# Optimization experiments

Hardware: AMD Instinct MI355X
Metric: run time of the kernel (lower is better)

The kernel has to match this reference:

```python
import jax, jax.numpy as jnp
import numpy as np
from jax import lax

B, T, E, H, V, D_ACT, OUT = 128, 512, 12, 512, 16, 10, 64


def setup_inputs() -> dict:
    key = jax.random.key(0)
    ks = jax.random.split(key, 9)
    ts = jax.random.uniform(ks[0], (B, T, 2), dtype=jnp.float32)
    idx = jax.random.randint(ks[1], (B, T), 0, V).astype(jnp.float32)
    x = jnp.concatenate([ts, idx[..., None]], axis=-1)  # [B,T,3], col2 = activity ids
    emb = jax.random.normal(ks[2], (V, D_ACT), jnp.float32) * 0.1
    emb = emb.at[0].set(0.0)  # padding_idx=0
    W_fwd = jax.random.normal(ks[3], (E, 3 * H), jnp.float32) / np.sqrt(E).astype(np.float32)
    b_fwd = jnp.zeros((3 * H,), jnp.float32)
    W_bwd = jax.random.normal(ks[4], (E, 3 * H), jnp.float32) / np.sqrt(E).astype(np.float32)
    b_bwd = jnp.zeros((3 * H,), jnp.float32)
    weight_Mu = jax.random.normal(ks[5], (2 * H, 1), jnp.float32) * 0.1
    W_out = jax.random.normal(ks[6], (OUT, 2 * H), jnp.float32) * 0.01  # torch Linear layout [out,in]
    b_out = jnp.zeros((OUT,), jnp.float32)
    return {"x": x, "emb": emb, "W_fwd": W_fwd, "b_fwd": b_fwd,
            "W_bwd": W_bwd, "b_bwd": b_bwd, "weight_Mu": weight_Mu,
            "W_out": W_out, "b_out": b_out}


def _fo_pool(z, f):
    # h_t = f_t * h_{t-1} + (1 - f_t) * z_t, scanned over time (axis 0)
    def step(c, zf):
        z_t, f_t = zf
        c = f_t * c + (1.0 - f_t) * z_t
        return c, c
    c0 = jnp.zeros_like(z[0])
    _, cs = lax.scan(step, c0, (z, f))
    return cs  # [T,B,H]


def _qrnn_dir(inp, W, b):
    # inp: [T,B,E] -> gates [T,B,3H]
    Y = inp @ W + b
    Z, F_, O = jnp.split(Y, 3, axis=-1)
    Z = jnp.tanh(Z)
    F_ = jax.nn.sigmoid(F_)
    O = jax.nn.sigmoid(O)
    C = _fo_pool(Z, F_)
    return O * C  # [T,B,H]


def reference(x, emb, W_fwd, b_fwd, W_bwd, b_bwd, weight_Mu, W_out, b_out):
    ts = x[:, :, :2]                                   # [B,T,2] time features
    act = emb[x[:, :, 2].astype(jnp.int32)]            # [B,T,10]
    enc = jnp.concatenate([ts, act], axis=-1)          # [B,T,E]
    inp = jnp.transpose(enc, (1, 0, 2))                # [T,B,E]
    h_f = _qrnn_dir(inp, W_fwd, b_fwd)                 # [T,B,H]
    h_b = _qrnn_dir(inp[::-1], W_bwd, b_bwd)[::-1]     # reverse-direction QRNN
    out = jnp.concatenate([h_f, h_b], axis=-1)         # [T,B,2H]
    out = jax.nn.relu(jnp.transpose(out, (1, 0, 2)))   # [B,T,2H]
    attn = jax.nn.softmax(out @ weight_Mu, axis=1)     # [B,T,1], softmax over time
    context = jnp.einsum('btd,bt->bd', out, attn[..., 0])  # [B,2H]
    context = jax.nn.relu(context)
    return context @ W_out.T + b_out                   # [B,OUT]
```

## Files before the change

kernel.cpp:

```cpp
#include <hip/hip_runtime.h>
#include <hip/hip_bf16.h>

#define B_   128
#define T_   512
#define H_   512
#define V_   16
#define OUT_ 64
#define DH_  1024


#define TAB_BYTES (V_*H_*16)
#define TSA_BYTES (T_*8)
#define VPK_BYTES (T_)
#define SCAN_LDS  (TAB_BYTES + TSA_BYTES + VPK_BYTES)

#define LOG2E 1.4426950408889634f

__device__ __forceinline__ float bf2f_lo(unsigned int u) {
    union { unsigned int i; float f; } x; x.i = u << 16; return x.f;
}
__device__ __forceinline__ float bf2f_hi(unsigned int u) {
    union { unsigned int i; float f; } x; x.i = u & 0xffff0000u; return x.f;
}

__global__ __launch_bounds__(512) void qrnn_scan8(
    const float* __restrict__ x,
    const float* __restrict__ emb,
    const float* __restrict__ Wf, const float* __restrict__ bf_,
    const float* __restrict__ Wb, const float* __restrict__ bb_,
    __hip_bfloat16* __restrict__ hbuf)
{
    const int b = blockIdx.x, dir = blockIdx.y, h = threadIdx.x;
    const float* __restrict__ W    = dir ? Wb  : Wf;
    const float* __restrict__ bias = dir ? bb_ : bf_;

    extern __shared__ char smem[];
    float4*        tab = (float4*)smem;
    float2*        tsA = (float2*)(smem + TAB_BYTES);
    unsigned char* vpk = (unsigned char*)(smem + TAB_BYTES + TSA_BYTES);

    {
        const int t = h;
        const float* xp = x + ((size_t)b*T_ + t)*3;
        tsA[t] = make_float2(xp[0], xp[1]);
        vpk[t] = (unsigned char)(int)xp[2];
    }

    float w0[3], w1[3], wt[10][3];
#pragma unroll
    for (int g = 0; g < 3; ++g) {
        w0[g] = W[g*H_ + h];
        w1[g] = W[1536 + g*H_ + h];
#pragma unroll
        for (int e = 0; e < 10; ++e)
            wt[e][g] = W[(2+e)*1536 + g*H_ + h];
    }
    const float bz = bias[h], bfv = bias[H_+h], bov = bias[2*H_+h];

    const float FZ = -2.8853900817779268f;
    const float FF = -1.4426950408889634f;

#pragma unroll
    for (int v = 0; v < V_; ++v) {
        float a0 = bz, a1 = bfv, a2 = bov;
#pragma unroll
        for (int e = 0; e < 10; ++e) {
            const float ev = emb[v*10 + e];
            a0 = fmaf(ev, wt[e][0], a0);
            a1 = fmaf(ev, wt[e][1], a1);
            a2 = fmaf(ev, wt[e][2], a2);
        }
        tab[v*H_ + h] = make_float4(FZ*a0, FF*a1, FF*a2, 0.f);
    }
    const float w0z = FZ*w0[0], w0f = FF*w0[1], w0o = FF*w0[2];
    const float w1z = FZ*w1[0], w1f = FF*w1[1], w1o = FF*w1[2];
    __syncthreads();

    const float4* tsA4 = (const float4*)tsA;
    const uint2*  vp2  = (const uint2*)vpk;

    float c = 0.f;
    __hip_bfloat16* hb = hbuf + (size_t)b*DH_ + dir*H_ + h;

#define SS(i, A0, A1, G) { \
    const float zp = fmaf(A0, w0z, fmaf(A1, w1z, (G).x)); \
    const float fp = fmaf(A0, w0f, fmaf(A1, w1f, (G).y)); \
    const float op = fmaf(A0, w0o, fmaf(A1, w1o, (G).z)); \
    const float Az = 1.f + __builtin_amdgcn_exp2f(zp); \
    const float Bf = 1.f + __builtin_amdgcn_exp2f(fp); \
    const float Co = 1.f + __builtin_amdgcn_exp2f(op); \
    const float AB = Az*Bf, BC = Bf*Co, AC = Az*Co; \
    const float r  = __builtin_amdgcn_rcpf(AB*Co); \
    const float f  = AC*r; \
    const float og = AB*r; \
    const float z  = (2.f - Az)*(BC*r); \
    c = fmaf(f, c - z, z); \
    const float hv = fmaxf(og * c, 0.f); \
    hb[(size_t)(t0 + (i))*(B_*DH_)] = __float2bfloat16(hv); \
}

#pragma unroll 2
    for (int gi = 0; gi < T_/8; ++gi) {
        const int gg = dir ? (T_/8 - 1 - gi) : gi;
        const int t0 = gg*8;
        const uint2  vp  = vp2[gg];
        const float4 tsa = tsA4[gg*4 + 0];
        const float4 tsb = tsA4[gg*4 + 1];
        const float4 tsc = tsA4[gg*4 + 2];
        const float4 tsd = tsA4[gg*4 + 3];
        const int v0 =  vp.x        & 255, v1 = (vp.x >> 8) & 255;
        const int v2 = (vp.x >> 16) & 255, v3 =  vp.x >> 24;
        const int v4 =  vp.y        & 255, v5 = (vp.y >> 8) & 255;
        const int v6 = (vp.y >> 16) & 255, v7 =  vp.y >> 24;
        const float4 g0 = tab[v0*H_ + h];
        const float4 g1 = tab[v1*H_ + h];
        const float4 g2 = tab[v2*H_ + h];
        const float4 g3 = tab[v3*H_ + h];
        const float4 g4 = tab[v4*H_ + h];
        const float4 g5 = tab[v5*H_ + h];
        const float4 g6 = tab[v6*H_ + h];
        const float4 g7 = tab[v7*H_ + h];
        if (dir == 0) {
            SS(0, tsa.x, tsa.y, g0) SS(1, tsa.z, tsa.w, g1)
            SS(2, tsb.x, tsb.y, g2) SS(3, tsb.z, tsb.w, g3)
            SS(4, tsc.x, tsc.y, g4) SS(5, tsc.z, tsc.w, g5)
            SS(6, tsd.x, tsd.y, g6) SS(7, tsd.z, tsd.w, g7)
        } else {
            SS(7, tsd.z, tsd.w, g7) SS(6, tsd.x, tsd.y, g6)
            SS(5, tsc.z, tsc.w, g5) SS(4, tsc.x, tsc.y, g4)
            SS(3, tsb.z, tsb.w, g3) SS(2, tsb.x, tsb.y, g2)
            SS(1, tsa.z, tsa.w, g1) SS(0, tsa.x, tsa.y, g0)
        }
    }
#undef SS
}

__global__ __launch_bounds__(1024) void postfuse(
    const __hip_bfloat16* __restrict__ hbuf,
    const float* __restrict__ Mu,
    const float* __restrict__ Wout,
    const float* __restrict__ bout,
    float* __restrict__ out)
{
    const int b    = blockIdx.x;
    const int w    = threadIdx.x >> 6;
    const int lane = threadIdx.x & 63;

    __shared__ float pw[16][DH_];
    __shared__ float psum[16];

    float mu[16];
    const float4* mp = (const float4*)Mu;
#pragma unroll
    for (int k = 0; k < 2; ++k) {
        const float4 m0 = mp[(k*64 + lane)*2];
        const float4 m1 = mp[(k*64 + lane)*2 + 1];
        mu[k*8+0]=m0.x; mu[k*8+1]=m0.y; mu[k*8+2]=m0.z; mu[k*8+3]=m0.w;
        mu[k*8+4]=m1.x; mu[k*8+5]=m1.y; mu[k*8+6]=m1.z; mu[k*8+7]=m1.w;
    }

    float acc[16];
#pragma unroll
    for (int i = 0; i < 16; ++i) acc[i] = 0.f;
    float esum = 0.f;

    for (int j = 0; j < T_/16; ++j) {
        const int t = j*16 + w;
        const uint4* hp = (const uint4*)(hbuf + ((size_t)t*B_ + b)*DH_);
        const uint4 u0 = hp[lane];
        const uint4 u1 = hp[64 + lane];
        float hv[16];
        hv[0]  = bf2f_lo(u0.x); hv[1]  = bf2f_hi(u0.x);
        hv[2]  = bf2f_lo(u0.y); hv[3]  = bf2f_hi(u0.y);
        hv[4]  = bf2f_lo(u0.z); hv[5]  = bf2f_hi(u0.z);
        hv[6]  = bf2f_lo(u0.w); hv[7]  = bf2f_hi(u0.w);
        hv[8]  = bf2f_lo(u1.x); hv[9]  = bf2f_hi(u1.x);
        hv[10] = bf2f_lo(u1.y); hv[11] = bf2f_hi(u1.y);
        hv[12] = bf2f_lo(u1.z); hv[13] = bf2f_hi(u1.z);
        hv[14] = bf2f_lo(u1.w); hv[15] = bf2f_hi(u1.w);

        float s = 0.f;
#pragma unroll
        for (int i = 0; i < 16; ++i) s = fmaf(hv[i], mu[i], s);
#pragma unroll
        for (int off = 1; off <= 32; off <<= 1) s += __shfl_xor(s, off);

        const float e = __builtin_amdgcn_exp2f(s * LOG2E);
        esum += e;
#pragma unroll
        for (int i = 0; i < 16; ++i) acc[i] = fmaf(hv[i], e, acc[i]);
    }

#pragma unroll
    for (int k = 0; k < 2; ++k) {
        *(float4*)&pw[w][k*512 + lane*8]     = make_float4(acc[k*8+0], acc[k*8+1], acc[k*8+2], acc[k*8+3]);
        *(float4*)&pw[w][k*512 + lane*8 + 4] = make_float4(acc[k*8+4], acc[k*8+5], acc[k*8+6], acc[k*8+7]);
    }
    if (lane == 0) psum[w] = esum;
    __syncthreads();

    {
        const int d = threadIdx.x;
        float cs = 0.f;
#pragma unroll
        for (int i = 0; i < 16; ++i) cs += pw[i][d];
        pw[0][d] = fmaxf(cs, 0.f);
    }
    float rsum = 0.f;
#pragma unroll
    for (int i = 0; i < 16; ++i) rsum += psum[i];
    const float rinv = __builtin_amdgcn_rcpf(rsum);
    __syncthreads();

#pragma unroll
    for (int oo = 0; oo < 4; ++oo) {
        const int o = w*4 + oo;
        const float* wp = Wout + o*DH_;
        float a = 0.f;
#pragma unroll
        for (int k = 0; k < 16; ++k) {
            const int d = k*64 + lane;
            a = fmaf(pw[0][d], wp[d], a);
        }
#pragma unroll
        for (int off = 1; off <= 32; off <<= 1) a += __shfl_xor(a, off);
        if (lane == 0) out[b*OUT_ + o] = a*rinv + bout[o];
    }
}

extern "C" void kernel_launch(void* const* d_in, const int* in_sizes, int n_in,
                              void* d_out, int out_size, void* d_ws, size_t ws_size,
                              hipStream_t stream)
{
    const float* x    = (const float*)d_in[0];
    const float* emb  = (const float*)d_in[1];
    const float* Wf   = (const float*)d_in[2];
    const float* bf_  = (const float*)d_in[3];
    const float* Wb   = (const float*)d_in[4];
    const float* bb_  = (const float*)d_in[5];
    const float* Mu   = (const float*)d_in[6];
    const float* Wout = (const float*)d_in[7];
    const float* bout = (const float*)d_in[8];
    float* out = (float*)d_out;

    __hip_bfloat16* hbuf = (__hip_bfloat16*)d_ws;

    (void)hipFuncSetAttribute((const void*)qrnn_scan8,
                              hipFuncAttributeMaxDynamicSharedMemorySize,
                              SCAN_LDS);

    qrnn_scan8<<<dim3(B_, 2), 512, SCAN_LDS, stream>>>(x, emb, Wf, bf_, Wb, bb_, hbuf);
    postfuse<<<B_, 1024, 0, stream>>>(hbuf, Mu, Wout, bout, out);
}
```

Before: 172.0 us.

## Split attention pooling over time chunks and simplify gate activations with rcp

The attention/context pooling kernel now runs on a (batch, 8 time-chunk) grid of 512-thread blocks instead of one 1024-thread block per batch. Each block writes partial context sums and exp sums to workspace, and a new combine kernel reduces them and applies the output projection. This targets the poor occupancy of the old 128-block pooling launch, at the cost of an extra kernel launch and a partial-sum round trip through global memory. The scan kernel also replaces the shared-reciprocal sigmoid/tanh formulation with three separate rcp calls, trading extra transcendental ops for fewer multiplies.

```diff
diff --git a/kernel.cpp b/kernel.cpp
--- a/kernel.cpp
+++ b/kernel.cpp
@@ -7,6 +7,7 @@
 #define V_   16
 #define OUT_ 64
 #define DH_  1024
+#define NCH  8
 
 
 #define TAB_BYTES (V_*H_*16)
@@ -23,7 +24,7 @@
     union { unsigned int i; float f; } x; x.i = u & 0xffff0000u; return x.f;
 }
 
-__global__ __launch_bounds__(512) void qrnn_scan8(
+__global__ __launch_bounds__(512) void qrnn_scan9(
     const float* __restrict__ x,
     const float* __restrict__ emb,
     const float* __restrict__ Wf, const float* __restrict__ bf_,
@@ -86,16 +87,12 @@
     const float zp = fmaf(A0, w0z, fmaf(A1, w1z, (G).x)); \
     const float fp = fmaf(A0, w0f, fmaf(A1, w1f, (G).y)); \
     const float op = fmaf(A0, w0o, fmaf(A1, w1o, (G).z)); \
-    const float Az = 1.f + __builtin_amdgcn_exp2f(zp); \
-    const float Bf = 1.f + __builtin_amdgcn_exp2f(fp); \
-    const float Co = 1.f + __builtin_amdgcn_exp2f(op); \
-    const float AB = Az*Bf, BC = Bf*Co, AC = Az*Co; \
-    const float r  = __builtin_amdgcn_rcpf(AB*Co); \
-    const float f  = AC*r; \
-    const float og = AB*r; \
-    const float z  = (2.f - Az)*(BC*r); \
+    const float rz = __builtin_amdgcn_rcpf(1.f + __builtin_amdgcn_exp2f(zp)); \
+    const float f  = __builtin_amdgcn_rcpf(1.f + __builtin_amdgcn_exp2f(fp)); \
+    const float o  = __builtin_amdgcn_rcpf(1.f + __builtin_amdgcn_exp2f(op)); \
+    const float z  = fmaf(2.f, rz, -1.f); \
     c = fmaf(f, c - z, z); \
-    const float hv = fmaxf(og * c, 0.f); \
+    const float hv = fmaxf(o * c, 0.f); \
     hb[(size_t)(t0 + (i))*(B_*DH_)] = __float2bfloat16(hv); \
 }
 
@@ -135,19 +132,19 @@
 #undef SS
 }
 
-__global__ __launch_bounds__(1024) void postfuse(
+__global__ __launch_bounds__(512) void postfuse2(
     const __hip_bfloat16* __restrict__ hbuf,
     const float* __restrict__ Mu,
-    const float* __restrict__ Wout,
-    const float* __restrict__ bout,
-    float* __restrict__ out)
+    float* __restrict__ pctx,
+    float* __restrict__ pesum)
 {
     const int b    = blockIdx.x;
+    const int q    = blockIdx.y;
     const int w    = threadIdx.x >> 6;
     const int lane = threadIdx.x & 63;
 
-    __shared__ float pw[16][DH_];
-    __shared__ float psum[16];
+    __shared__ float pw[8][DH_];
+    __shared__ float psum[8];
 
     float mu[16];
     const float4* mp = (const float4*)Mu;
@@ -164,8 +161,9 @@
     for (int i = 0; i < 16; ++i) acc[i] = 0.f;
     float esum = 0.f;
 
-    for (int j = 0; j < T_/16; ++j) {
-        const int t = j*16 + w;
+#pragma unroll 2
+    for (int j = 0; j < 8; ++j) {
+        const int t = q*64 + j*8 + w;
         const uint4* hp = (const uint4*)(hbuf + ((size_t)t*B_ + b)*DH_);
         const uint4 u0 = hp[lane];
         const uint4 u1 = hp[64 + lane];
@@ -201,26 +199,62 @@
 
     {
         const int d = threadIdx.x;
-        float cs = 0.f;
-#pragma unroll
-        for (int i = 0; i < 16; ++i) cs += pw[i][d];
-        pw[0][d] = fmaxf(cs, 0.f);
-    }
-    float rsum = 0.f;
-#pragma unroll
-    for (int i = 0; i < 16; ++i) rsum += psum[i];
-    const float rinv = __builtin_amdgcn_rcpf(rsum);
+        float c0 = 0.f, c1 = 0.f;
+#pragma unroll
+        for (int i = 0; i < 8; ++i) { c0 += pw[i][d]; c1 += pw[i][d + 512]; }
+        float* pc = pctx + ((size_t)b*NCH + q)*DH_;
+        pc[d]       = c0;
+        pc[d + 512] = c1;
+    }
+    if (threadIdx.x == 0) {
+        float ts = 0.f;
+#pragma unroll
+        for (int i = 0; i < 8; ++i) ts += psum[i];
+        pesum[b*NCH + q] = ts;
+    }
+}
+
+__global__ __launch_bounds__(512) void combine_out(
+    const float* __restrict__ pctx,
+    const float* __restrict__ pesum,
+    const float* __restrict__ Wout,
+    const float* __restrict__ bout,
+    float* __restrict__ out)
+{
+    const int b    = blockIdx.x;
+    const int w    = threadIdx.x >> 6;
+    const int lane = threadIdx.x & 63;
+
+    __shared__ float ctx[DH_];
+    __shared__ float rinv_s;
+
+    {
+        const int d = threadIdx.x;
+        const float* pc = pctx + (size_t)b*NCH*DH_;
+        float c0 = 0.f, c1 = 0.f;
+#pragma unroll
+        for (int i = 0; i < NCH; ++i) { c0 += pc[i*DH_ + d]; c1 += pc[i*DH_ + d + 512]; }
+        ctx[d]       = fmaxf(c0, 0.f);
+        ctx[d + 512] = fmaxf(c1, 0.f);
+    }
+    if (threadIdx.x == 0) {
+        float ts = 0.f;
+#pragma unroll
+        for (int i = 0; i < NCH; ++i) ts += pesum[b*NCH + i];
+        rinv_s = __builtin_amdgcn_rcpf(ts);
+    }
     __syncthreads();
 
-#pragma unroll
-    for (int oo = 0; oo < 4; ++oo) {
-        const int o = w*4 + oo;
+    const float rinv = rinv_s;
+#pragma unroll
+    for (int oo = 0; oo < 8; ++oo) {
+        const int o = w*8 + oo;
         const float* wp = Wout + o*DH_;
         float a = 0.f;
 #pragma unroll
         for (int k = 0; k < 16; ++k) {
             const int d = k*64 + lane;
-            a = fmaf(pw[0][d], wp[d], a);
+            a = fmaf(ctx[d], wp[d], a);
         }
 #pragma unroll
         for (int off = 1; off <= 32; off <<= 1) a += __shfl_xor(a, off);
@@ -243,12 +277,17 @@
     const float* bout = (const float*)d_in[8];
     float* out = (float*)d_out;
 
-    __hip_bfloat16* hbuf = (__hip_bfloat16*)d_ws;
-
-    (void)hipFuncSetAttribute((const void*)qrnn_scan8,
+    char* ws = (char*)d_ws;
+    const size_t hbytes = (size_t)B_*T_*DH_*sizeof(__hip_bfloat16);
+    __hip_bfloat16* hbuf = (__hip_bfloat16*)ws;
+    float* pctx  = (float*)(ws + hbytes);
+    float* pesum = pctx + (size_t)B_*NCH*DH_;
+
+    (void)hipFuncSetAttribute((const void*)qrnn_scan9,
                               hipFuncAttributeMaxDynamicSharedMemorySize,
                               SCAN_LDS);
 
-    qrnn_scan8<<<dim3(B_, 2), 512, SCAN_LDS, stream>>>(x, emb, Wf, bf_, Wb, bb_, hbuf);
-    postfuse<<<B_, 1024, 0, stream>>>(hbuf, Mu, Wout, bout, out);
-}
+    qrnn_scan9<<<dim3(B_, 2), 512, SCAN_LDS, stream>>>(x, emb, Wf, bf_, Wb, bb_, hbuf);
+    postfuse2<<<dim3(B_, NCH), 512, 0, stream>>>(hbuf, Mu, pctx, pesum);
+    combine_out<<<B_, 512, 0, stream>>>(pctx, pesum, Wout, bout, out);
+}
```

After: 170.3 us. About the same (-1.0%).
